# Kernel optimization log

Measured on AMD Instinct MI355X. Metric: run time of the kernel, lower is better.

Reference implementation:

```python
import jax, jax.numpy as jnp
import numpy as np
import math


def _per_component_log_likelihood(x, MU, A, D, PI):
    # x: [N,d]; MU,D: [K,d]; A: [K,d,l]; PI: [K]
    K, d, l = A.shape
    iD = D ** (-2.0)                                   # [K,d]  (1/sigma^2 per feature)
    B = iD[:, :, None] * A                             # [K,d,l] = diag(iD_k) @ A_k
    # L_k = I_l + A_k^T diag(iD_k) A_k  (Woodbury inner matrix)
    L = jnp.eye(l, dtype=x.dtype)[None] + jnp.einsum('kdl,kdm->klm', A, B)
    iL = jnp.linalg.inv(L)                             # [K,l,l]
    # Mahalanobis term m_d[n,k] = xc^T iD xc - (xc^T iD A) iL (A^T iD xc),
    # expanded so we never materialize the [K,N,d] centered tensor.
    t_quad = (x * x) @ iD.T                            # [N,K]
    t_cross = x @ (iD * MU).T                          # [N,K]
    t_const = jnp.sum(iD * MU * MU, axis=1)            # [K]
    term1 = t_quad - 2.0 * t_cross + t_const[None, :]
    y = jnp.einsum('nd,kdl->nkl', x, B) - jnp.einsum('kd,kdl->kl', MU, B)[None]
    term2 = jnp.einsum('nkl,klm,nkm->nk', y, iL, y)
    m_d = term1 - term2                                # [N,K]
    # log|Sigma_k| = log|L_k| - sum_d log iD[k,d]
    log_det_Sigma = jnp.log(jnp.linalg.det(L)) + jnp.sum(jnp.log(D ** 2.0), axis=1)
    log_prob = -0.5 * ((d * math.log(2.0 * math.pi) + log_det_Sigma)[None, :] + m_d)
    # NOTE: faithful to the source, which adds PI (not log PI) here.
    return PI[None, :] + log_prob                      # [N,K]


def setup_inputs() -> dict:
    key = jax.random.key(0)
    k1, k2, k3, k4 = jax.random.split(key, 4)
    N, K, d, l = 500000, 32, 128, 4
    x = jax.random.normal(k1, (N, d), dtype=jnp.float32)
    MU = jax.random.normal(k2, (K, d), dtype=jnp.float32)
    A = 0.1 * jax.random.normal(k3, (K, d, l), dtype=jnp.float32)
    D = jax.random.uniform(k4, (K, d), dtype=jnp.float32, minval=0.5, maxval=1.5)
    PI = jnp.ones((K,), dtype=jnp.float32) / K
    return {"x": x, "MU": MU, "A": A, "D": D, "PI": PI}


def reference(x, MU, A, D, PI):
    comp_ll = _per_component_log_likelihood(x, MU, A, D, PI)   # [N,K]
    return jax.scipy.special.logsumexp(comp_ll, axis=1)        # [N] = MFA.log_prob(x)
```

## Files before the change

kernel.cpp:

```cpp
#include <hip/hip_runtime.h>
#include <hip/hip_bf16.h>

typedef _Float16 half8  __attribute__((ext_vector_type(8)));
typedef _Float16 half2v __attribute__((ext_vector_type(2)));
typedef float    f32x16 __attribute__((ext_vector_type(16)));

#define KC 32
#define DD 128
#define LL 4
#define NCOL 192
#define NBLK 768
#define WPB 4
#define NSLOT (NBLK*WPB)

__global__ __launch_bounds__(256) void mfa_woodbury(
    const float* __restrict__ MU, const float* __restrict__ A,
    const float* __restrict__ D, const float* __restrict__ PI,
    float* __restrict__ wsc, float* __restrict__ wsh, float* __restrict__ wsr)
{
  __shared__ float sPart[KC][8][16];
  const int tid = threadIdx.x;
  const int k = tid >> 3;
  const int sub = tid & 7;

  {
    float p[16];
#pragma unroll
    for (int i = 0; i < 16; ++i) p[i] = 0.f;
    const int d0 = sub * 16;
#pragma unroll 4
    for (int di = 0; di < 16; ++di) {
      const int d = d0 + di;
      const float Dv = D[k*DD + d];
      const float id = 1.0f/(Dv*Dv);
      const float mu = MU[k*DD + d];
      float a[LL];
#pragma unroll
      for (int l = 0; l < LL; ++l) a[l] = A[(k*DD + d)*LL + l];
      int s = 0;
#pragma unroll
      for (int l = 0; l < LL; ++l) {
#pragma unroll
        for (int m2 = 0; m2 <= l; ++m2) { p[s] += a[l]*id*a[m2]; ++s; }
        p[10 + l] += mu*id*a[l];
      }
      p[14] += id*mu*mu;
      p[15] += __logf(Dv*Dv);
    }
#pragma unroll
    for (int i = 0; i < 16; ++i) sPart[k][sub][i] = p[i];
  }
  __syncthreads();

  if (tid < KC) {
    const int kk = tid;
    float p[16];
#pragma unroll
    for (int i = 0; i < 16; ++i) p[i] = 0.f;
    for (int s = 0; s < 8; ++s)
#pragma unroll
      for (int i = 0; i < 16; ++i) p[i] += sPart[kk][s][i];

    float Lm[LL][LL];
    {
      int s = 0;
      for (int l = 0; l < LL; ++l)
        for (int m2 = 0; m2 <= l; ++m2) { Lm[l][m2] = p[s]; ++s; }
    }
    for (int l = 0; l < LL; ++l) Lm[l][l] += 1.0f;
    float c[LL];
    for (int l = 0; l < LL; ++l) c[l] = p[10 + l];
    const float t_const  = p[14];
    const float sumlogD2 = p[15];

    float Lo[LL][LL];
    for (int i = 0; i < LL; ++i)
      for (int j = 0; j < LL; ++j) Lo[i][j] = 0.f;
    for (int i = 0; i < LL; ++i) {
      float s = Lm[i][i];
      for (int m2 = 0; m2 < i; ++m2) s -= Lo[i][m2]*Lo[i][m2];
      Lo[i][i] = sqrtf(s);
      for (int j = i + 1; j < LL; ++j) {
        float t = Lm[j][i];
        for (int m2 = 0; m2 < i; ++m2) t -= Lo[j][m2]*Lo[i][m2];
        Lo[j][i] = t / Lo[i][i];
      }
    }
    float Ri[LL][LL];
    for (int i = 0; i < LL; ++i)
      for (int j = 0; j < LL; ++j) Ri[i][j] = 0.f;
    for (int i = 0; i < LL; ++i) {
      Ri[i][i] = 1.0f/Lo[i][i];
      for (int j = 0; j < i; ++j) {
        float s = 0.f;
        for (int m2 = j; m2 < i; ++m2) s += Lo[i][m2]*Ri[m2][j];
        Ri[i][j] = -s / Lo[i][i];
      }
    }
    for (int i = 0; i < LL; ++i)
      for (int j = 0; j < LL; ++j) wsr[kk*16 + i*4 + j] = Ri[i][j];
    for (int l = 0; l < LL; ++l) {
      float s = 0.f;
      for (int m2 = 0; m2 <= l; ++m2) s += Ri[l][m2]*c[m2];
      wsh[kk*LL + l] = s;
    }
    float logdetL = 0.f;
    for (int i = 0; i < LL; ++i) logdetL += __logf(Lo[i][i]);
    logdetL *= 2.0f;
    const float dlog2pi = 235.24826473f;
    wsc[kk] = PI[kk] - 0.5f*(dlog2pi + logdetL + sumlogD2) - 0.5f*t_const;
  }
}

__global__ __launch_bounds__(256) void mfa_weights(
    const float* __restrict__ MU, const float* __restrict__ A,
    const float* __restrict__ D, const float* __restrict__ wsr,
    _Float16* __restrict__ wsw)
{
  const int idx = (int)blockIdx.x*256 + (int)threadIdx.x;
  const int j    = idx & 7;
  const int lane = (idx >> 3) & 63;
  const int s    = (idx >> 9) & 7;
  const int t    = idx >> 12;
  const int col  = t*32 + (lane & 31);
  const int dd   = s*16 + ((lane >> 5) << 3) + j;
  float v;
  if (col < 32) {
    const float Dv = D[col*DD + dd];
    v = 1.0f/(Dv*Dv);
  } else if (col < 64) {
    const int kk = col - 32;
    const float Dv = D[kk*DD + dd];
    v = MU[kk*DD + dd]/(Dv*Dv);
  } else {
    const int kk = (col - 64) >> 2, l = (col - 64) & 3;
    const float Dv = D[kk*DD + dd];
    const float id = 1.0f/(Dv*Dv);
    float s2 = 0.f;
    for (int m2 = 0; m2 <= l; ++m2)
      s2 += A[(kk*DD + dd)*LL + m2] * wsr[kk*16 + l*4 + m2];
    v = id*s2;
  }
  wsw[idx] = (_Float16)v;
}

__device__ inline half2v pkrtz(float a, float b) {
  return __builtin_bit_cast(half2v, __builtin_amdgcn_cvt_pkrtz(a, b));
}
__device__ inline half2v shx2(half2v v, int d) {
  int i = __builtin_bit_cast(int, v);
  i = __shfl_xor(i, d);
  return __builtin_bit_cast(half2v, i);
}
__device__ inline half2v shl2(half2v v, int src) {
  int i = __builtin_bit_cast(int, v);
  i = __shfl(i, src);
  return __builtin_bit_cast(half2v, i);
}
template <int CTRL>
__device__ inline half2v dpp2(half2v v) {
  int i = __builtin_bit_cast(int, v);
  int r = __builtin_amdgcn_update_dpp(i, i, CTRL, 0xF, 0xF, true);
  return __builtin_bit_cast(half2v, r);
}
__device__ inline half2v pmax2(half2v a, half2v b) {
  half2v r;
  r[0] = a[0] > b[0] ? a[0] : b[0];
  r[1] = a[1] > b[1] ? a[1] : b[1];
  return r;
}
__device__ inline half2v sel8(const half2v* p, int i) {
  half2v a = (i & 1) ? p[1] : p[0];
  half2v b = (i & 1) ? p[3] : p[2];
  half2v c = (i & 1) ? p[5] : p[4];
  half2v d = (i & 1) ? p[7] : p[6];
  half2v e = (i & 2) ? b : a;
  half2v f = (i & 2) ? d : c;
  return (i & 4) ? f : e;
}

__global__ __launch_bounds__(256, 3) void mfa_main(
    const float* __restrict__ x, const _Float16* __restrict__ wsw,
    const float* __restrict__ wsc, const float* __restrict__ wsh,
    float* __restrict__ out, int N, int ntiles, int iters)
{
  __shared__ int4 sWbuf[3072];
  const int tid = threadIdx.x;
  {
    const int4* src = (const int4*)wsw;
    for (int i = tid; i < 3072; i += 256) sWbuf[i] = src[i];
  }
  const half8* sW8 = (const half8*)sWbuf;

  const int wv = tid >> 6, lane = tid & 63;
  const int c = lane & 31;
  const int h = lane >> 5;
  const float cc = wsc[c];
  float hz[4];
#pragma unroll
  for (int zt = 0; zt < 4; ++zt) hz[zt] = wsh[(8*zt + (c >> 2))*4 + (c & 3)];
  const int srcl = (lane & 32) | ((c & 7) << 2) | (c & 3);

  __syncthreads();

  for (int it = 0; it < iters; ++it) {
    const int tile = it*NSLOT + (int)blockIdx.x*WPB + wv;
    if (tile >= ntiles) continue;

    int row = tile*32 + c;
    if (row >= N) row = N - 1;
    const float* xr = x + (size_t)row*DD + h*8;

    f32x16 acc[6];
#pragma unroll
    for (int t = 0; t < 6; ++t)
#pragma unroll
      for (int r = 0; r < 16; ++r) acc[t][r] = 0.f;

#pragma unroll
    for (int half_b = 0; half_b < 2; ++half_b) {
      float4 xv[8];
#pragma unroll
      for (int s = 0; s < 4; ++s) {
        const int ss = half_b*4 + s;
        xv[2*s]     = *(const float4*)(xr + ss*16);
        xv[2*s + 1] = *(const float4*)(xr + ss*16 + 4);
      }
#pragma unroll
      for (int s = 0; s < 4; ++s) {
        const int ss = half_b*4 + s;
        const float4 a = xv[2*s], b = xv[2*s + 1];
        union { half8 v; half2v p[4]; } hx, hx2;
        hx.p[0] = pkrtz(a.x, a.y);
        hx.p[1] = pkrtz(a.z, a.w);
        hx.p[2] = pkrtz(b.x, b.y);
        hx.p[3] = pkrtz(b.z, b.w);
        hx2.v = hx.v * hx.v;
        acc[0] = __builtin_amdgcn_mfma_f32_32x32x16_f16(
            hx2.v, sW8[(0*8 + ss)*64 + lane], acc[0], 0, 0, 0);
#pragma unroll
        for (int t = 1; t < 6; ++t)
          acc[t] = __builtin_amdgcn_mfma_f32_32x32x16_f16(
              hx.v, sW8[(t*8 + ss)*64 + lane], acc[t], 0, 0, 0);
      }
    }

    float vp[16];
#pragma unroll
    for (int r = 0; r < 16; ++r)
      vp[r] = acc[1][r] - 0.5f*acc[0][r] + cc;

    half2v tq[4][8];
#pragma unroll
    for (int zt = 0; zt < 4; ++zt)
#pragma unroll
      for (int i = 0; i < 8; ++i) {
        const float e0 = acc[2 + zt][2*i]     - hz[zt];
        const float e1 = acc[2 + zt][2*i + 1] - hz[zt];
        half2v p = pkrtz(e0*e0, e1*e1);
        p = p + dpp2<0xB1>(p);
        p = p + dpp2<0x4E>(p);
        tq[zt][i] = p;
      }
#pragma unroll
    for (int i = 0; i < 8; ++i) {
      half2v b0 = shl2(tq[0][i], srcl);
      half2v b1 = shl2(tq[1][i], srcl);
      half2v b2 = shl2(tq[2][i], srcl);
      half2v b3 = shl2(tq[3][i], srcl);
      half2v m01 = (c & 8)  ? b1 : b0;
      half2v m23 = (c & 8)  ? b3 : b2;
      half2v st  = (c & 16) ? m23 : m01;
      vp[2*i]     += 0.5f*(float)st[0];
      vp[2*i + 1] += 0.5f*(float)st[1];
    }

    half2v pm[8];
#pragma unroll
    for (int i = 0; i < 8; ++i)
      pm[i] = pkrtz(vp[2*i], vp[2*i + 1]);
#pragma unroll
    for (int i = 0; i < 8; ++i) {
      pm[i] = pmax2(pm[i], dpp2<0xB1>(pm[i]));
      pm[i] = pmax2(pm[i], dpp2<0x4E>(pm[i]));
      pm[i] = pmax2(pm[i], dpp2<0x141>(pm[i]));
      pm[i] = pmax2(pm[i], dpp2<0x140>(pm[i]));
      pm[i] = pmax2(pm[i], shx2(pm[i], 16));
    }

    half2v ps[8];
#pragma unroll
    for (int i = 0; i < 8; ++i) {
      const float e0 = __expf(vp[2*i]     - (float)pm[i][0]);
      const float e1 = __expf(vp[2*i + 1] - (float)pm[i][1]);
      ps[i] = pkrtz(e0, e1);
    }
#pragma unroll
    for (int i = 0; i < 8; ++i) {
      ps[i] = ps[i] + dpp2<0xB1>(ps[i]);
      ps[i] = ps[i] + dpp2<0x4E>(ps[i]);
      ps[i] = ps[i] + dpp2<0x141>(ps[i]);
      ps[i] = ps[i] + dpp2<0x140>(ps[i]);
      ps[i] = ps[i] + shx2(ps[i], 16);
    }

    if (c < 16) {
      const half2v S = sel8(ps, c >> 1);
      const half2v M = sel8(pm, c >> 1);
      const float sum = (c & 1) ? (float)S[1] : (float)S[0];
      const float mx  = (c & 1) ? (float)M[1] : (float)M[0];
      const int rw = tile*32 + (c & 3) + 8*(c >> 2) + 4*h;
      if (rw < N) out[rw] = mx + __logf(sum);
    }
  }
}

extern "C" void kernel_launch(void* const* d_in, const int* in_sizes, int n_in,
                              void* d_out, int out_size, void* d_ws, size_t ws_size,
                              hipStream_t stream) {
  const float* x  = (const float*)d_in[0];
  const float* MU = (const float*)d_in[1];
  const float* A  = (const float*)d_in[2];
  const float* D  = (const float*)d_in[3];
  const float* PI = (const float*)d_in[4];
  float* out = (float*)d_out;

  const int N = in_sizes[0] / DD;
  _Float16* wsw = (_Float16*)d_ws;
  float* wsc = (float*)((char*)d_ws + (size_t)NCOL*DD*sizeof(_Float16));
  float* wsh = wsc + KC;
  float* wsr = wsh + KC*LL;

  hipLaunchKernelGGL(mfa_woodbury, dim3(1), dim3(256), 0, stream,
                     MU, A, D, PI, wsc, wsh, wsr);
  hipLaunchKernelGGL(mfa_weights, dim3(96), dim3(256), 0, stream,
                     MU, A, D, wsr, wsw);

  const int ntiles = (N + 31) / 32;
  const int iters  = (ntiles + NSLOT - 1) / NSLOT;
  hipLaunchKernelGGL(mfa_main, dim3(NBLK), dim3(256), 0, stream,
                     x, wsw, wsc, wsh, out, N, ntiles, iters);
}
```

Before: 370.7 us.

## Fuse Woodbury precompute and weight packing into main kernel

Drops the two preprocessing kernels and instead has every block of the main kernel compute the per-component Cholesky, inverse, constants and fp16 weight matrix itself, writing them straight into shared memory. This removes two extra kernel launches and the serial dependency and workspace round-trip through global memory. In exchange, all 768 blocks repeat the same small precompute (reading MU, A and D, with a few syncs) before they start streaming x.

Result: no change. 370.3 us (-0.1%).

```diff
diff --git a/kernel.cpp b/kernel.cpp
--- a/kernel.cpp
+++ b/kernel.cpp
@@ -8,35 +8,76 @@
 #define KC 32
 #define DD 128
 #define LL 4
-#define NCOL 192
 #define NBLK 768
 #define WPB 4
 #define NSLOT (NBLK*WPB)
 
-__global__ __launch_bounds__(256) void mfa_woodbury(
-    const float* __restrict__ MU, const float* __restrict__ A,
-    const float* __restrict__ D, const float* __restrict__ PI,
-    float* __restrict__ wsc, float* __restrict__ wsh, float* __restrict__ wsr)
+__device__ inline half2v pkrtz(float a, float b) {
+  return __builtin_bit_cast(half2v, __builtin_amdgcn_cvt_pkrtz(a, b));
+}
+__device__ inline half2v shx2(half2v v, int d) {
+  int i = __builtin_bit_cast(int, v);
+  i = __shfl_xor(i, d);
+  return __builtin_bit_cast(half2v, i);
+}
+__device__ inline half2v shl2(half2v v, int src) {
+  int i = __builtin_bit_cast(int, v);
+  i = __shfl(i, src);
+  return __builtin_bit_cast(half2v, i);
+}
+template <int CTRL>
+__device__ inline half2v dpp2(half2v v) {
+  int i = __builtin_bit_cast(int, v);
+  int r = __builtin_amdgcn_update_dpp(i, i, CTRL, 0xF, 0xF, true);
+  return __builtin_bit_cast(half2v, r);
+}
+__device__ inline half2v pmax2(half2v a, half2v b) {
+  half2v r;
+  r[0] = a[0] > b[0] ? a[0] : b[0];
+  r[1] = a[1] > b[1] ? a[1] : b[1];
+  return r;
+}
+__device__ inline half2v sel8(const half2v* p, int i) {
+  half2v a = (i & 1) ? p[1] : p[0];
+  half2v b = (i & 1) ? p[3] : p[2];
+  half2v c = (i & 1) ? p[5] : p[4];
+  half2v d = (i & 1) ? p[7] : p[6];
+  half2v e = (i & 2) ? b : a;
+  half2v f = (i & 2) ? d : c;
+  return (i & 4) ? f : e;
+}
+
+__global__ __launch_bounds__(256, 3) void mfa_fused(
+    const float* __restrict__ x, const float* __restrict__ MU,
+    const float* __restrict__ A, const float* __restrict__ D,
+    const float* __restrict__ PI, float* __restrict__ out,
+    int N, int ntiles, int iters)
 {
-  __shared__ float sPart[KC][8][16];
+  __shared__ int4 sWbuf[3072];
+  __shared__ float sMeta[672];
+  float* sMetaR = sMeta;
+  float* sMetaH = sMeta + 512;
+  float* sMetaC = sMeta + 640;
+
   const int tid = threadIdx.x;
-  const int k = tid >> 3;
+  const int k   = tid >> 3;
   const int sub = tid & 7;
-
+  const int dbase = k*DD + sub*16;
+
+  float idv[16], muv[16];
   {
+    float (*sPart)[8][16] = (float (*)[8][16])sWbuf;
     float p[16];
 #pragma unroll
     for (int i = 0; i < 16; ++i) p[i] = 0.f;
-    const int d0 = sub * 16;
-#pragma unroll 4
+#pragma unroll
     for (int di = 0; di < 16; ++di) {
-      const int d = d0 + di;
-      const float Dv = D[k*DD + d];
+      const float Dv = D[dbase + di];
       const float id = 1.0f/(Dv*Dv);
-      const float mu = MU[k*DD + d];
-      float a[LL];
-#pragma unroll
-      for (int l = 0; l < LL; ++l) a[l] = A[(k*DD + d)*LL + l];
+      const float mu = MU[dbase + di];
+      idv[di] = id; muv[di] = mu;
+      const float4 a4 = *(const float4*)(A + (size_t)(dbase + di)*LL);
+      const float a[LL] = {a4.x, a4.y, a4.z, a4.w};
       int s = 0;
 #pragma unroll
       for (int l = 0; l < LL; ++l) {
@@ -53,6 +94,7 @@
   __syncthreads();
 
   if (tid < KC) {
+    float (*sPart)[8][16] = (float (*)[8][16])sWbuf;
     const int kk = tid;
     float p[16];
 #pragma unroll
@@ -68,8 +110,8 @@
         for (int m2 = 0; m2 <= l; ++m2) { Lm[l][m2] = p[s]; ++s; }
     }
     for (int l = 0; l < LL; ++l) Lm[l][l] += 1.0f;
-    float c[LL];
-    for (int l = 0; l < LL; ++l) c[l] = p[10 + l];
+    float cv[LL];
+    for (int l = 0; l < LL; ++l) cv[l] = p[10 + l];
     const float t_const  = p[14];
     const float sumlogD2 = p[15];
 
@@ -98,110 +140,70 @@
       }
     }
     for (int i = 0; i < LL; ++i)
-      for (int j = 0; j < LL; ++j) wsr[kk*16 + i*4 + j] = Ri[i][j];
+      for (int j = 0; j < LL; ++j) sMetaR[kk*16 + i*4 + j] = Ri[i][j];
     for (int l = 0; l < LL; ++l) {
       float s = 0.f;
-      for (int m2 = 0; m2 <= l; ++m2) s += Ri[l][m2]*c[m2];
-      wsh[kk*LL + l] = s;
+      for (int m2 = 0; m2 <= l; ++m2) s += Ri[l][m2]*cv[m2];
+      sMetaH[kk*LL + l] = s;
     }
     float logdetL = 0.f;
     for (int i = 0; i < LL; ++i) logdetL += __logf(Lo[i][i]);
     logdetL *= 2.0f;
     const float dlog2pi = 235.24826473f;
-    wsc[kk] = PI[kk] - 0.5f*(dlog2pi + logdetL + sumlogD2) - 0.5f*t_const;
+    sMetaC[kk] = PI[kk] - 0.5f*(dlog2pi + logdetL + sumlogD2) - 0.5f*t_const;
   }
-}
-
-__global__ __launch_bounds__(256) void mfa_weights(
-    const float* __restrict__ MU, const float* __restrict__ A,
-    const float* __restrict__ D, const float* __restrict__ wsr,
-    _Float16* __restrict__ wsw)
-{
-  const int idx = (int)blockIdx.x*256 + (int)threadIdx.x;
-  const int j    = idx & 7;
-  const int lane = (idx >> 3) & 63;
-  const int s    = (idx >> 9) & 7;
-  const int t    = idx >> 12;
-  const int col  = t*32 + (lane & 31);
-  const int dd   = s*16 + ((lane >> 5) << 3) + j;
-  float v;
-  if (col < 32) {
-    const float Dv = D[col*DD + dd];
-    v = 1.0f/(Dv*Dv);
-  } else if (col < 64) {
-    const int kk = col - 32;
-    const float Dv = D[kk*DD + dd];
-    v = MU[kk*DD + dd]/(Dv*Dv);
-  } else {
-    const int kk = (col - 64) >> 2, l = (col - 64) & 3;
-    const float Dv = D[kk*DD + dd];
-    const float id = 1.0f/(Dv*Dv);
-    float s2 = 0.f;
-    for (int m2 = 0; m2 <= l; ++m2)
-      s2 += A[(kk*DD + dd)*LL + m2] * wsr[kk*16 + l*4 + m2];
-    v = id*s2;
+  __syncthreads();
+
+  {
+    float Rm[LL][LL];
+#pragma unroll
+    for (int l = 0; l < LL; ++l)
+#pragma unroll
+      for (int m = 0; m < LL; ++m) Rm[l][m] = sMetaR[k*16 + l*4 + m];
+    half8* sW8w = (half8*)sWbuf;
+#pragma unroll
+    for (int h2 = 0; h2 < 2; ++h2) {
+      half8 vq, vr, vz0, vz1, vz2, vz3;
+#pragma unroll
+      for (int j = 0; j < 8; ++j) {
+        const int di = 8*h2 + j;
+        const float id = idv[di];
+        const float mu = muv[di];
+        const float4 a4 = *(const float4*)(A + (size_t)(dbase + di)*LL);
+        vq[j] = (_Float16)id;
+        vr[j] = (_Float16)(id*mu);
+        const float s0 = a4.x*Rm[0][0];
+        const float s1 = a4.x*Rm[1][0] + a4.y*Rm[1][1];
+        const float s2 = a4.x*Rm[2][0] + a4.y*Rm[2][1] + a4.z*Rm[2][2];
+        const float s3 = a4.x*Rm[3][0] + a4.y*Rm[3][1] + a4.z*Rm[3][2]
+                       + a4.w*Rm[3][3];
+        vz0[j] = (_Float16)(id*s0);
+        vz1[j] = (_Float16)(id*s1);
+        vz2[j] = (_Float16)(id*s2);
+        vz3[j] = (_Float16)(id*s3);
+      }
+      const int lq = (h2 << 5) | k;
+      sW8w[(0*8 + sub)*64 + lq] = vq;
+      sW8w[(1*8 + sub)*64 + lq] = vr;
+      const int tz = 2 + (k >> 3);
+      const int lz = (h2 << 5) | ((k & 7) << 2);
+      sW8w[(tz*8 + sub)*64 + lz + 0] = vz0;
+      sW8w[(tz*8 + sub)*64 + lz + 1] = vz1;
+      sW8w[(tz*8 + sub)*64 + lz + 2] = vz2;
+      sW8w[(tz*8 + sub)*64 + lz + 3] = vz3;
+    }
   }
-  wsw[idx] = (_Float16)v;
-}
-
-__device__ inline half2v pkrtz(float a, float b) {
-  return __builtin_bit_cast(half2v, __builtin_amdgcn_cvt_pkrtz(a, b));
-}
-__device__ inline half2v shx2(half2v v, int d) {
-  int i = __builtin_bit_cast(int, v);
-  i = __shfl_xor(i, d);
-  return __builtin_bit_cast(half2v, i);
-}
-__device__ inline half2v shl2(half2v v, int src) {
-  int i = __builtin_bit_cast(int, v);
-  i = __shfl(i, src);
-  return __builtin_bit_cast(half2v, i);
-}
-template <int CTRL>
-__device__ inline half2v dpp2(half2v v) {
-  int i = __builtin_bit_cast(int, v);
-  int r = __builtin_amdgcn_update_dpp(i, i, CTRL, 0xF, 0xF, true);
-  return __builtin_bit_cast(half2v, r);
-}
-__device__ inline half2v pmax2(half2v a, half2v b) {
-  half2v r;
-  r[0] = a[0] > b[0] ? a[0] : b[0];
-  r[1] = a[1] > b[1] ? a[1] : b[1];
-  return r;
-}
-__device__ inline half2v sel8(const half2v* p, int i) {
-  half2v a = (i & 1) ? p[1] : p[0];
-  half2v b = (i & 1) ? p[3] : p[2];
-  half2v c = (i & 1) ? p[5] : p[4];
-  half2v d = (i & 1) ? p[7] : p[6];
-  half2v e = (i & 2) ? b : a;
-  half2v f = (i & 2) ? d : c;
-  return (i & 4) ? f : e;
-}
-
-__global__ __launch_bounds__(256, 3) void mfa_main(
-    const float* __restrict__ x, const _Float16* __restrict__ wsw,
-    const float* __restrict__ wsc, const float* __restrict__ wsh,
-    float* __restrict__ out, int N, int ntiles, int iters)
-{
-  __shared__ int4 sWbuf[3072];
-  const int tid = threadIdx.x;
-  {
-    const int4* src = (const int4*)wsw;
-    for (int i = tid; i < 3072; i += 256) sWbuf[i] = src[i];
-  }
+  __syncthreads();
+
   const half8* sW8 = (const half8*)sWbuf;
-
   const int wv = tid >> 6, lane = tid & 63;
   const int c = lane & 31;
   const int h = lane >> 5;
-  const float cc = wsc[c];
+  const float cc = sMetaC[c];
   float hz[4];
 #pragma unroll
-  for (int zt = 0; zt < 4; ++zt) hz[zt] = wsh[(8*zt + (c >> 2))*4 + (c & 3)];
+  for (int zt = 0; zt < 4; ++zt) hz[zt] = sMetaH[(8*zt + (c >> 2))*4 + (c & 3)];
   const int srcl = (lane & 32) | ((c & 7) << 2) | (c & 3);
-
-  __syncthreads();
 
   for (int it = 0; it < iters; ++it) {
     const int tile = it*NSLOT + (int)blockIdx.x*WPB + wv;
@@ -318,6 +320,7 @@
 extern "C" void kernel_launch(void* const* d_in, const int* in_sizes, int n_in,
                               void* d_out, int out_size, void* d_ws, size_t ws_size,
                               hipStream_t stream) {
+  (void)n_in; (void)out_size; (void)d_ws; (void)ws_size;
   const float* x  = (const float*)d_in[0];
   const float* MU = (const float*)d_in[1];
   const float* A  = (const float*)d_in[2];
@@ -326,18 +329,8 @@
   float* out = (float*)d_out;
 
   const int N = in_sizes[0] / DD;
-  _Float16* wsw = (_Float16*)d_ws;
-  float* wsc = (float*)((char*)d_ws + (size_t)NCOL*DD*sizeof(_Float16));
-  float* wsh = wsc + KC;
-  float* wsr = wsh + KC*LL;
-
-  hipLaunchKernelGGL(mfa_woodbury, dim3(1), dim3(256), 0, stream,
-                     MU, A, D, PI, wsc, wsh, wsr);
-  hipLaunchKernelGGL(mfa_weights, dim3(96), dim3(256), 0, stream,
-                     MU, A, D, wsr, wsw);
-
   const int ntiles = (N + 31) / 32;
   const int iters  = (ntiles + NSLOT - 1) / NSLOT;
-  hipLaunchKernelGGL(mfa_main, dim3(NBLK), dim3(256), 0, stream,
-                     x, wsw, wsc, wsh, out, N, ntiles, iters);
-}
+  hipLaunchKernelGGL(mfa_fused, dim3(NBLK), dim3(256), 0, stream,
+                     x, MU, A, D, PI, out, N, ntiles, iters);
+}
```
